# Optimization experiments

Hardware: AMD Instinct MI355X
Metric: run time of the kernel (lower is better)

Reference implementation:

```python
import jax, jax.numpy as jnp
import numpy as np

B, C, T, V, H = 64, 256, 64, 25, 512


def setup_inputs() -> dict:
    key = jax.random.key(0)
    k_h, k_w1, k_w2, k_r = jax.random.split(key, 4)
    h = jax.random.normal(k_h, (B, C, T, V), dtype=jnp.float32)
    W1 = jax.random.normal(k_w1, (C, H), dtype=jnp.float32) * 0.02
    b1 = jnp.zeros((H,), dtype=jnp.float32)
    W2 = jax.random.normal(k_w2, (H, C), dtype=jnp.float32) * 0.02
    b2 = jnp.zeros((C,), dtype=jnp.float32)
    # per-step teacher-forcing uniforms, one per (timestep, batch elem)
    tf_rand = jax.random.uniform(k_r, (T - 1, B), dtype=jnp.float32)
    return {"h": h, "W1": W1, "b1": b1, "W2": W2, "b2": b2,
            "tf_rand": tf_rand, "t_obs": 16}


def reference(h, W1, b1, W2, b2, tf_rand, t_obs):
    # training=True, run_backwards=False branch of ODEEulerSolver.forward
    # ode_func: 2-layer MLP over the channel dim (time index unused)
    def ode(z):  # z: [B, C, V]
        u = jnp.tanh(jnp.einsum('bcv,ch->bhv', z, W1) + b1[None, :, None])
        return jnp.einsum('bhv,hc->bcv', u, W2) + b2[None, :, None]

    z0 = h[:, :, 0, :]                           # [B, C, V]
    h_prev = jnp.moveaxis(h[:, :, :-1, :], 2, 0)  # [T-1, B, C, V] teacher states

    def step(z_prev, inp):
        h_t, r = inp                              # h_t: [B,C,V], r: [B]
        # rand < 0.5 -> keep previous prediction, else teacher-force h[:, :, t-1]
        mask = (r < 0.5)[:, None, None]
        z_t = jnp.where(mask, z_prev, h_t)
        z_next = z_t + ode(z_t)                   # Euler step
        return z_next, z_next

    _, zs = jax.lax.scan(step, z0, (h_prev, tf_rand))  # zs: [T-1, B, C, V]
    z_hat = jnp.concatenate([z0[:, :, None, :], jnp.moveaxis(zs, 0, 2)], axis=2)
    return z_hat  # [B, C, T, V]
```

## Files before the change

kernel.cpp:

```cpp
#include <hip/hip_runtime.h>
#include <hip/hip_bf16.h>
#include <math.h>


using bf16x8 = __attribute__((ext_vector_type(8))) short;
using f32x4  = __attribute__((ext_vector_type(4))) float;

constexpr int Bb = 64, Cc = 256, Tt = 64, Vv = 25, Hh = 512;
constexpr int TV = Tt * Vv;
constexpr int MAXCH = Bb * (Tt - 1);
constexpr int NGRID = 2496;
constexpr int NTMAX = 4;

__device__ __forceinline__ short f2bf(float x) {
  union { float f; unsigned u; } v; v.f = x;
  unsigned r = v.u + 0x7FFFu + ((v.u >> 16) & 1u);
  return (short)(r >> 16);
}
__device__ __forceinline__ float fast_tanh(float x) {
  float e = __expf(2.f * x);
  return 1.f - 2.f * __builtin_amdgcn_rcpf(e + 1.f);
}
__device__ __forceinline__ void bar_lds() {
  asm volatile("s_waitcnt lgkmcnt(0)" ::: "memory");
  __builtin_amdgcn_s_barrier();
  asm volatile("" ::: "memory");
}
__device__ __forceinline__ void gl2lds16(const short* g, short* l) {
  __builtin_amdgcn_global_load_lds(
      (const __attribute__((address_space(1))) void*)g,
      (__attribute__((address_space(3))) void*)l, 16, 0, 0);
}

__global__ void prep_kernel(const float* __restrict__ W1,
                            const float* __restrict__ W2,
                            const float* __restrict__ tf,
                            short* __restrict__ a1p,
                            short* __restrict__ a2p,
                            int* __restrict__ sorted,
                            int* __restrict__ hdr) {
  if (blockIdx.x < 1024) {
    int idx = blockIdx.x * 256 + threadIdx.x;
    if (idx < 131072) {
      int j = idx & 7, lane = (idx >> 3) & 63, mt = (idx >> 9) & 31, kt = idx >> 14;
      int h = mt * 16 + (lane & 15);
      int c = kt * 32 + (lane >> 4) * 8 + j;
      a1p[idx] = f2bf(W1[c * Hh + h]);
    } else {
      int i2 = idx - 131072;
      int j = i2 & 7, lane = (i2 >> 3) & 63, mt = (i2 >> 9) & 15, kt = i2 >> 13;
      int cm = mt * 16 + (lane & 15);
      int hk = kt * 32 + (lane >> 4) * 8 + j;
      a2p[i2] = f2bf(W2[hk * Cc + cm]);
    }
    return;
  }
  __shared__ int cnt[64];
  __shared__ int ofs[64];
  int tid = threadIdx.x;
  if (tid < 64) cnt[tid] = 0;
  for (int i = tid; i < MAXCH; i += 256) sorted[i] = 0;
  __syncthreads();
  if (tid < Bb) {
    int b = tid, prev = 0;
    for (int t = 1; t <= 62; t++)
      if (tf[t * Bb + b] >= 0.5f) { atomicAdd(&cnt[t - prev], 1); prev = t; }
    atomicAdd(&cnt[63 - prev], 1);
  }
  __syncthreads();
  if (tid == 0) {
    int acc = 0;
    for (int l = 63; l >= 1; l--) { ofs[l] = acc; acc += cnt[l]; }
    int n1 = 0;
    for (int l = 5; l <= 63; l++) n1 += cnt[l];
    hdr[0] = n1;
    hdr[1] = (acc - n1 + 1) >> 1;
    hdr[2] = acc; hdr[3] = 0;
  }
  __syncthreads();
  if (tid < Bb) {
    int b = tid, prev = 0;
    for (int t = 1; t <= 62; t++) {
      if (tf[t * Bb + b] >= 0.5f) {
        int len = t - prev;
        int p = atomicAdd(&ofs[len], 1);
        sorted[p] = b | (prev << 6) | (len << 12);
        prev = t;
      }
    }
    int len = 63 - prev;
    int p = atomicAdd(&ofs[len], 1);
    sorted[p] = b | (prev << 6) | (len << 12);
  }
}

template<int NCH>
__device__ __forceinline__ void run_group(
    int start,
    const float* __restrict__ hsrc, const float* __restrict__ b1,
    const float* __restrict__ b2,   const short* __restrict__ a1p,
    const short* __restrict__ a2p,  const int* __restrict__ sorted,
    float* __restrict__ out, short* __restrict__ zB, short* __restrict__ uB,
    short* __restrict__ wA) {
  constexpr int NTA = NCH * 2;
  const int tid  = threadIdx.x;
  const int lane = tid & 63;
  const int w    = tid >> 6;
  const int m16  = lane & 15;
  const int quad = lane >> 4;
  short* wv = wA + w * 4096;

  int meta[NCH], len[NCH], sbase[NCH], t0s[NCH];
  #pragma unroll
  for (int j = 0; j < NCH; j++) {
    meta[j]  = sorted[start + j];
    len[j]   = (meta[j] >> 12) & 63;
    t0s[j]   = (meta[j] >> 6) & 63;
    sbase[j] = (meta[j] & 63) * Cc * TV + t0s[j] * Vv;
  }
  const int maxlen = len[0];

  bf16x8 w1r[2][8][2];
  #pragma unroll
  for (int ch = 0; ch < 2; ch++)
    #pragma unroll
    for (int kt = 0; kt < 8; kt++) {
      const short* ab = a1p + ((kt * 32 + ch * 16 + w * 2) * 64 + lane) * 8;
      w1r[ch][kt][0] = *(const bf16x8*)ab;
      w1r[ch][kt][1] = *(const bf16x8*)(ab + 512);
    }

  f32x4 acc2[2][NTA];

  #pragma unroll
  for (int i = 0; i < 2; i++) {
    const int cbase = (w * 2 + i) * 16 + quad * 4;
    const int ktz = cbase >> 5;
    const int gq  = (cbase >> 3) & 3;
    const int j0  = cbase & 7;
    #pragma unroll
    for (int nt = 0; nt < NTA; nt++) {
      const int j  = nt >> 1;
      const int v  = (nt & 1) * 16 + m16;
      const bool valid = (len[j] > 0) && (v < Vv);
      const int hb = sbase[j] + cbase * TV + v;
      f32x4 z;
      #pragma unroll
      for (int r = 0; r < 4; r++)
        z[r] = valid ? __builtin_nontemporal_load(&hsrc[hb + r * TV]) : 0.f;
      acc2[i][nt] = z;
      short4 zh;
      zh.x = f2bf(z[0]); zh.y = f2bf(z[1]); zh.z = f2bf(z[2]); zh.w = f2bf(z[3]);
      *(short4*)&zB[((ktz * NTMAX + nt) * 64 + m16 + 16 * gq) * 8 + j0] = zh;
      if (valid && t0s[j] == 0) {
        #pragma unroll
        for (int r = 0; r < 4; r++) out[hb + r * TV] = z[r];
      }
    }
  }

  auto ISSUE = [&](int tile) {
    const short* gp = a2p + ((tile * 16 + w * 2) * 64 + lane) * 8;
    short* lp = wv + (tile & 3) * 1024;
    gl2lds16(gp, lp);
    gl2lds16(gp + 512, lp + 512);
  };

  ISSUE(0);
  ISSUE(1);
  bar_lds();

  f32x4 b2v[2];
  f32x4 b1v[2][2];
  #pragma unroll
  for (int i = 0; i < 2; i++) {
    const float4 t = *(const float4*)(b2 + (w * 2 + i) * 16 + quad * 4);
    b2v[i] = (f32x4){t.x, t.y, t.z, t.w};
    #pragma unroll
    for (int ch = 0; ch < 2; ch++) {
      const float4 u = *(const float4*)(b1 + ch * 256 + (w * 2 + i) * 16 + quad * 4);
      b1v[ch][i] = (f32x4){u.x, u.y, u.z, u.w};
    }
  }

  for (int s = 0; s < maxlen; s++) {
    auto MM1R = [&](int ch, f32x4 (&a1)[2][NTA]) {
      #pragma unroll
      for (int kt = 0; kt < 8; kt++) {
        #pragma unroll
        for (int nt = 0; nt < NTA; nt++) {
          bf16x8 bz = *(const bf16x8*)&zB[((kt * NTMAX + nt) * 64 + lane) * 8];
          a1[0][nt] = __builtin_amdgcn_mfma_f32_16x16x32_bf16(w1r[ch][kt][0], bz, a1[0][nt], 0, 0, 0);
          a1[1][nt] = __builtin_amdgcn_mfma_f32_16x16x32_bf16(w1r[ch][kt][1], bz, a1[1][nt], 0, 0, 0);
        }
      }
    };
    auto MM2R = [&](int ch) {
      #pragma unroll
      for (int kt = 0; kt < 8; kt++) {
        const int tile = ch * 8 + kt;
        ISSUE((tile + 2) & 15);
        asm volatile("s_waitcnt vmcnt(4)" ::: "memory");
        const short* wp = wv + (tile & 3) * 1024 + lane * 8;
        bf16x8 af0 = *(const bf16x8*)wp;
        bf16x8 af1 = *(const bf16x8*)(wp + 512);
        #pragma unroll
        for (int nt = 0; nt < NTA; nt++) {
          bf16x8 bu = *(const bf16x8*)&uB[((kt * NTMAX + nt) * 64 + lane) * 8];
          acc2[0][nt] = __builtin_amdgcn_mfma_f32_16x16x32_bf16(af0, bu, acc2[0][nt], 0, 0, 0);
          acc2[1][nt] = __builtin_amdgcn_mfma_f32_16x16x32_bf16(af1, bu, acc2[1][nt], 0, 0, 0);
        }
      }
    };
    auto UEPI = [&](int ch, f32x4 (&a1)[2][NTA]) {
      #pragma unroll
      for (int i = 0; i < 2; i++) {
        const int hl  = (w * 2 + i) * 16 + quad * 4;
        const int ktl = hl >> 5;
        const int gq  = (hl >> 3) & 3;
        const int j0  = hl & 7;
        #pragma unroll
        for (int nt = 0; nt < NTA; nt++) {
          short4 up;
          up.x = f2bf(fast_tanh(a1[i][nt][0] + b1v[ch][i][0]));
          up.y = f2bf(fast_tanh(a1[i][nt][1] + b1v[ch][i][1]));
          up.z = f2bf(fast_tanh(a1[i][nt][2] + b1v[ch][i][2]));
          up.w = f2bf(fast_tanh(a1[i][nt][3] + b1v[ch][i][3]));
          *(short4*)&uB[((ktl * NTMAX + nt) * 64 + m16 + 16 * gq) * 8 + j0] = up;
        }
      }
    };

    #pragma unroll
    for (int i = 0; i < 2; i++)
      #pragma unroll
      for (int nt = 0; nt < NTA; nt++) {
        acc2[i][nt][0] += b2v[i][0]; acc2[i][nt][1] += b2v[i][1];
        acc2[i][nt][2] += b2v[i][2]; acc2[i][nt][3] += b2v[i][3];
      }

    f32x4 acc1[2][NTA];
    #pragma unroll
    for (int i = 0; i < 2; i++)
      #pragma unroll
      for (int nt = 0; nt < NTA; nt++) acc1[i][nt] = (f32x4){0.f, 0.f, 0.f, 0.f};
    MM1R(0, acc1);
    UEPI(0, acc1);
    bar_lds();
    MM2R(0);
    #pragma unroll
    for (int i = 0; i < 2; i++)
      #pragma unroll
      for (int nt = 0; nt < NTA; nt++) acc1[i][nt] = (f32x4){0.f, 0.f, 0.f, 0.f};
    MM1R(1, acc1);
    bar_lds();
    UEPI(1, acc1);
    bar_lds();
    MM2R(1);
    #pragma unroll
    for (int i = 0; i < 2; i++) {
      const int cbase = (w * 2 + i) * 16 + quad * 4;
      const int ktz = cbase >> 5;
      const int gq  = (cbase >> 3) & 3;
      const int j0  = cbase & 7;
      #pragma unroll
      for (int nt = 0; nt < NTA; nt++) {
        short4 zh;
        zh.x = f2bf(acc2[i][nt][0]); zh.y = f2bf(acc2[i][nt][1]);
        zh.z = f2bf(acc2[i][nt][2]); zh.w = f2bf(acc2[i][nt][3]);
        *(short4*)&zB[((ktz * NTMAX + nt) * 64 + m16 + 16 * gq) * 8 + j0] = zh;
        const int v = (nt & 1) * 16 + m16;
        if (v < Vv && s < len[nt >> 1]) {
          const int o = sbase[nt >> 1] + cbase * TV + v + (s + 1) * Vv;
          out[o]          = acc2[i][nt][0];
          out[o + TV]     = acc2[i][nt][1];
          out[o + 2 * TV] = acc2[i][nt][2];
          out[o + 3 * TV] = acc2[i][nt][3];
        }
      }
    }
    bar_lds();
  }
}

__global__ __launch_bounds__(512, 2) void group_kernel(
    const float* __restrict__ hsrc, const float* __restrict__ b1,
    const float* __restrict__ b2,   const short* __restrict__ a1p,
    const short* __restrict__ a2p,  const int* __restrict__ sorted,
    const int* __restrict__ hdr,    float* __restrict__ out) {
  __shared__ __align__(16) short zB[8 * NTMAX * 64 * 8];
  __shared__ __align__(16) short uB[8 * NTMAX * 64 * 8];
  __shared__ __align__(16) short wA[8 * 4 * 1024];

  const int n1 = hdr[0], npair = hdr[1];
  const int bi = blockIdx.x;
  if (bi < n1) {
    run_group<1>(bi, hsrc, b1, b2, a1p, a2p, sorted, out, zB, uB, wA);
  } else if (bi < n1 + npair) {
    run_group<2>(n1 + (bi - n1) * 2, hsrc, b1, b2, a1p, a2p, sorted, out, zB, uB, wA);
  }
}

extern "C" void kernel_launch(void* const* d_in, const int* in_sizes, int n_in,
                              void* d_out, int out_size, void* d_ws, size_t ws_size,
                              hipStream_t stream) {
  const float* h_ptr = (const float*)d_in[0];
  const float* W1    = (const float*)d_in[1];
  const float* b1    = (const float*)d_in[2];
  const float* W2    = (const float*)d_in[3];
  const float* b2    = (const float*)d_in[4];
  const float* tf    = (const float*)d_in[5];
  float* out = (float*)d_out;

  short* a1p  = (short*)d_ws;
  short* a2p  = a1p + 131072;
  int* sorted = (int*)(a2p + 131072);
  int* hdr    = sorted + MAXCH;

  prep_kernel<<<1025, 256, 0, stream>>>(W1, W2, tf, a1p, a2p, sorted, hdr);
  group_kernel<<<NGRID, 512, 0, stream>>>(h_ptr, b1, b2, a1p, a2p, sorted, hdr, out);
}
```

Measured before the change: 440.0 us.

## Stream W1/W2 fragments from global into registers, single-pass hidden layer

Drops the register-resident W1 fragments and the LDS ring buffer filled by global_load_lds for W2. Both weight matrices are now streamed straight from global/L2 into registers with one-k-tile-ahead prefetch on every step. The hidden layer is computed in one pass: each wave does all four 16-row H tiles, and the full 512-wide tanh output goes into a doubled uB buffer, which removes a barrier-separated chunk. This cuts register pressure and shrinks LDS use, but adds repeated global weight loads on every Euler step.

```diff
diff --git a/kernel.cpp b/kernel.cpp
--- a/kernel.cpp
+++ b/kernel.cpp
@@ -25,11 +25,6 @@
   asm volatile("s_waitcnt lgkmcnt(0)" ::: "memory");
   __builtin_amdgcn_s_barrier();
   asm volatile("" ::: "memory");
-}
-__device__ __forceinline__ void gl2lds16(const short* g, short* l) {
-  __builtin_amdgcn_global_load_lds(
-      (const __attribute__((address_space(1))) void*)g,
-      (__attribute__((address_space(3))) void*)l, 16, 0, 0);
 }
 
 __global__ void prep_kernel(const float* __restrict__ W1,
@@ -100,15 +95,13 @@
     const float* __restrict__ hsrc, const float* __restrict__ b1,
     const float* __restrict__ b2,   const short* __restrict__ a1p,
     const short* __restrict__ a2p,  const int* __restrict__ sorted,
-    float* __restrict__ out, short* __restrict__ zB, short* __restrict__ uB,
-    short* __restrict__ wA) {
+    float* __restrict__ out, short* __restrict__ zB, short* __restrict__ uB) {
   constexpr int NTA = NCH * 2;
   const int tid  = threadIdx.x;
   const int lane = tid & 63;
   const int w    = tid >> 6;
   const int m16  = lane & 15;
   const int quad = lane >> 4;
-  short* wv = wA + w * 4096;
 
   int meta[NCH], len[NCH], sbase[NCH], t0s[NCH];
   #pragma unroll
@@ -120,15 +113,18 @@
   }
   const int maxlen = len[0];
 
-  bf16x8 w1r[2][8][2];
-  #pragma unroll
-  for (int ch = 0; ch < 2; ch++)
-    #pragma unroll
-    for (int kt = 0; kt < 8; kt++) {
-      const short* ab = a1p + ((kt * 32 + ch * 16 + w * 2) * 64 + lane) * 8;
-      w1r[ch][kt][0] = *(const bf16x8*)ab;
-      w1r[ch][kt][1] = *(const bf16x8*)(ab + 512);
-    }
+  auto LDW1 = [&](int kt, bf16x8 (&f)[4]) {
+    const short* ab = a1p + ((kt * 32 + w * 4) * 64 + lane) * 8;
+    f[0] = *(const bf16x8*)ab;
+    f[1] = *(const bf16x8*)(ab + 512);
+    f[2] = *(const bf16x8*)(ab + 1024);
+    f[3] = *(const bf16x8*)(ab + 1536);
+  };
+  auto LDW2 = [&](int kt, bf16x8 (&f)[2]) {
+    const short* ab = a2p + ((kt * 16 + w * 2) * 64 + lane) * 8;
+    f[0] = *(const bf16x8*)ab;
+    f[1] = *(const bf16x8*)(ab + 512);
+  };
 
   f32x4 acc2[2][NTA];
 
@@ -159,104 +155,110 @@
     }
   }
 
-  auto ISSUE = [&](int tile) {
-    const short* gp = a2p + ((tile * 16 + w * 2) * 64 + lane) * 8;
-    short* lp = wv + (tile & 3) * 1024;
-    gl2lds16(gp, lp);
-    gl2lds16(gp + 512, lp + 512);
-  };
-
-  ISSUE(0);
-  ISSUE(1);
-  bar_lds();
+  bf16x8 w1k0[4], w2k0[2];
+  LDW1(0, w1k0);
+  LDW2(0, w2k0);
 
   f32x4 b2v[2];
-  f32x4 b1v[2][2];
+  f32x4 b1v[4];
   #pragma unroll
   for (int i = 0; i < 2; i++) {
     const float4 t = *(const float4*)(b2 + (w * 2 + i) * 16 + quad * 4);
     b2v[i] = (f32x4){t.x, t.y, t.z, t.w};
-    #pragma unroll
-    for (int ch = 0; ch < 2; ch++) {
-      const float4 u = *(const float4*)(b1 + ch * 256 + (w * 2 + i) * 16 + quad * 4);
-      b1v[ch][i] = (f32x4){u.x, u.y, u.z, u.w};
-    }
-  }
+  }
+  #pragma unroll
+  for (int i = 0; i < 4; i++) {
+    const float4 u = *(const float4*)(b1 + (w * 4 + i) * 16 + quad * 4);
+    b1v[i] = (f32x4){u.x, u.y, u.z, u.w};
+  }
+
+  bar_lds();
 
   for (int s = 0; s < maxlen; s++) {
-    auto MM1R = [&](int ch, f32x4 (&a1)[2][NTA]) {
-      #pragma unroll
-      for (int kt = 0; kt < 8; kt++) {
+    #pragma unroll
+    for (int i = 0; i < 2; i++)
+      #pragma unroll
+      for (int nt = 0; nt < NTA; nt++) {
+        acc2[i][nt][0] += b2v[i][0]; acc2[i][nt][1] += b2v[i][1];
+        acc2[i][nt][2] += b2v[i][2]; acc2[i][nt][3] += b2v[i][3];
+      }
+
+    f32x4 acc1[4][NTA];
+    #pragma unroll
+    for (int i = 0; i < 4; i++)
+      #pragma unroll
+      for (int nt = 0; nt < NTA; nt++) acc1[i][nt] = (f32x4){0.f, 0.f, 0.f, 0.f};
+
+    {
+      bf16x8 nA[4];
+      LDW1(1, nA);
+      #pragma unroll
+      for (int nt = 0; nt < NTA; nt++) {
+        bf16x8 bz = *(const bf16x8*)&zB[((0 * NTMAX + nt) * 64 + lane) * 8];
+        acc1[0][nt] = __builtin_amdgcn_mfma_f32_16x16x32_bf16(w1k0[0], bz, acc1[0][nt], 0, 0, 0);
+        acc1[1][nt] = __builtin_amdgcn_mfma_f32_16x16x32_bf16(w1k0[1], bz, acc1[1][nt], 0, 0, 0);
+        acc1[2][nt] = __builtin_amdgcn_mfma_f32_16x16x32_bf16(w1k0[2], bz, acc1[2][nt], 0, 0, 0);
+        acc1[3][nt] = __builtin_amdgcn_mfma_f32_16x16x32_bf16(w1k0[3], bz, acc1[3][nt], 0, 0, 0);
+      }
+      #pragma unroll
+      for (int kt = 1; kt < 8; kt++) {
+        bf16x8 cA[4];
+        #pragma unroll
+        for (int i = 0; i < 4; i++) cA[i] = nA[i];
+        if (kt < 7) LDW1(kt + 1, nA);
         #pragma unroll
         for (int nt = 0; nt < NTA; nt++) {
           bf16x8 bz = *(const bf16x8*)&zB[((kt * NTMAX + nt) * 64 + lane) * 8];
-          a1[0][nt] = __builtin_amdgcn_mfma_f32_16x16x32_bf16(w1r[ch][kt][0], bz, a1[0][nt], 0, 0, 0);
-          a1[1][nt] = __builtin_amdgcn_mfma_f32_16x16x32_bf16(w1r[ch][kt][1], bz, a1[1][nt], 0, 0, 0);
+          acc1[0][nt] = __builtin_amdgcn_mfma_f32_16x16x32_bf16(cA[0], bz, acc1[0][nt], 0, 0, 0);
+          acc1[1][nt] = __builtin_amdgcn_mfma_f32_16x16x32_bf16(cA[1], bz, acc1[1][nt], 0, 0, 0);
+          acc1[2][nt] = __builtin_amdgcn_mfma_f32_16x16x32_bf16(cA[2], bz, acc1[2][nt], 0, 0, 0);
+          acc1[3][nt] = __builtin_amdgcn_mfma_f32_16x16x32_bf16(cA[3], bz, acc1[3][nt], 0, 0, 0);
         }
       }
-    };
-    auto MM2R = [&](int ch) {
-      #pragma unroll
-      for (int kt = 0; kt < 8; kt++) {
-        const int tile = ch * 8 + kt;
-        ISSUE((tile + 2) & 15);
-        asm volatile("s_waitcnt vmcnt(4)" ::: "memory");
-        const short* wp = wv + (tile & 3) * 1024 + lane * 8;
-        bf16x8 af0 = *(const bf16x8*)wp;
-        bf16x8 af1 = *(const bf16x8*)(wp + 512);
+    }
+
+    #pragma unroll
+    for (int i = 0; i < 4; i++) {
+      const int hl  = (w * 4 + i) * 16 + quad * 4;
+      const int ktl = hl >> 5;
+      const int gq  = (hl >> 3) & 3;
+      const int j0  = hl & 7;
+      #pragma unroll
+      for (int nt = 0; nt < NTA; nt++) {
+        short4 up;
+        up.x = f2bf(fast_tanh(acc1[i][nt][0] + b1v[i][0]));
+        up.y = f2bf(fast_tanh(acc1[i][nt][1] + b1v[i][1]));
+        up.z = f2bf(fast_tanh(acc1[i][nt][2] + b1v[i][2]));
+        up.w = f2bf(fast_tanh(acc1[i][nt][3] + b1v[i][3]));
+        *(short4*)&uB[((ktl * NTMAX + nt) * 64 + m16 + 16 * gq) * 8 + j0] = up;
+      }
+    }
+
+    bar_lds();
+
+    {
+      bf16x8 nA[2];
+      LDW2(1, nA);
+      #pragma unroll
+      for (int nt = 0; nt < NTA; nt++) {
+        bf16x8 bu = *(const bf16x8*)&uB[((0 * NTMAX + nt) * 64 + lane) * 8];
+        acc2[0][nt] = __builtin_amdgcn_mfma_f32_16x16x32_bf16(w2k0[0], bu, acc2[0][nt], 0, 0, 0);
+        acc2[1][nt] = __builtin_amdgcn_mfma_f32_16x16x32_bf16(w2k0[1], bu, acc2[1][nt], 0, 0, 0);
+      }
+      #pragma unroll
+      for (int kt = 1; kt < 16; kt++) {
+        bf16x8 cA[2];
+        cA[0] = nA[0]; cA[1] = nA[1];
+        if (kt < 15) LDW2(kt + 1, nA);
         #pragma unroll
         for (int nt = 0; nt < NTA; nt++) {
           bf16x8 bu = *(const bf16x8*)&uB[((kt * NTMAX + nt) * 64 + lane) * 8];
-          acc2[0][nt] = __builtin_amdgcn_mfma_f32_16x16x32_bf16(af0, bu, acc2[0][nt], 0, 0, 0);
-          acc2[1][nt] = __builtin_amdgcn_mfma_f32_16x16x32_bf16(af1, bu, acc2[1][nt], 0, 0, 0);
+          acc2[0][nt] = __builtin_amdgcn_mfma_f32_16x16x32_bf16(cA[0], bu, acc2[0][nt], 0, 0, 0);
+          acc2[1][nt] = __builtin_amdgcn_mfma_f32_16x16x32_bf16(cA[1], bu, acc2[1][nt], 0, 0, 0);
         }
       }
-    };
-    auto UEPI = [&](int ch, f32x4 (&a1)[2][NTA]) {
-      #pragma unroll
-      for (int i = 0; i < 2; i++) {
-        const int hl  = (w * 2 + i) * 16 + quad * 4;
-        const int ktl = hl >> 5;
-        const int gq  = (hl >> 3) & 3;
-        const int j0  = hl & 7;
-        #pragma unroll
-        for (int nt = 0; nt < NTA; nt++) {
-          short4 up;
-          up.x = f2bf(fast_tanh(a1[i][nt][0] + b1v[ch][i][0]));
-          up.y = f2bf(fast_tanh(a1[i][nt][1] + b1v[ch][i][1]));
-          up.z = f2bf(fast_tanh(a1[i][nt][2] + b1v[ch][i][2]));
-          up.w = f2bf(fast_tanh(a1[i][nt][3] + b1v[ch][i][3]));
-          *(short4*)&uB[((ktl * NTMAX + nt) * 64 + m16 + 16 * gq) * 8 + j0] = up;
-        }
-      }
-    };
-
-    #pragma unroll
-    for (int i = 0; i < 2; i++)
-      #pragma unroll
-      for (int nt = 0; nt < NTA; nt++) {
-        acc2[i][nt][0] += b2v[i][0]; acc2[i][nt][1] += b2v[i][1];
-        acc2[i][nt][2] += b2v[i][2]; acc2[i][nt][3] += b2v[i][3];
-      }
-
-    f32x4 acc1[2][NTA];
-    #pragma unroll
-    for (int i = 0; i < 2; i++)
-      #pragma unroll
-      for (int nt = 0; nt < NTA; nt++) acc1[i][nt] = (f32x4){0.f, 0.f, 0.f, 0.f};
-    MM1R(0, acc1);
-    UEPI(0, acc1);
-    bar_lds();
-    MM2R(0);
-    #pragma unroll
-    for (int i = 0; i < 2; i++)
-      #pragma unroll
-      for (int nt = 0; nt < NTA; nt++) acc1[i][nt] = (f32x4){0.f, 0.f, 0.f, 0.f};
-    MM1R(1, acc1);
-    bar_lds();
-    UEPI(1, acc1);
-    bar_lds();
-    MM2R(1);
+    }
+
     #pragma unroll
     for (int i = 0; i < 2; i++) {
       const int cbase = (w * 2 + i) * 16 + quad * 4;
@@ -289,15 +291,14 @@
     const short* __restrict__ a2p,  const int* __restrict__ sorted,
     const int* __restrict__ hdr,    float* __restrict__ out) {
   __shared__ __align__(16) short zB[8 * NTMAX * 64 * 8];
-  __shared__ __align__(16) short uB[8 * NTMAX * 64 * 8];
-  __shared__ __align__(16) short wA[8 * 4 * 1024];
+  __shared__ __align__(16) short uB[16 * NTMAX * 64 * 8];
 
   const int n1 = hdr[0], npair = hdr[1];
   const int bi = blockIdx.x;
   if (bi < n1) {
-    run_group<1>(bi, hsrc, b1, b2, a1p, a2p, sorted, out, zB, uB, wA);
+    run_group<1>(bi, hsrc, b1, b2, a1p, a2p, sorted, out, zB, uB);
   } else if (bi < n1 + npair) {
-    run_group<2>(n1 + (bi - n1) * 2, hsrc, b1, b2, a1p, a2p, sorted, out, zB, uB, wA);
+    run_group<2>(n1 + (bi - n1) * 2, hsrc, b1, b2, a1p, a2p, sorted, out, zB, uB);
   }
 }
 
```

After: 498.9 us. +13.4%, slower.
